# Kernel tuning notes

Measured on AMD Instinct MI355X. Metric: run time of the kernel, lower is better.

The kernel has to match this reference:

```python
import jax, jax.numpy as jnp
import numpy as np

D, N_EXP, N_TOK = 2048, 8, 32768


def setup_inputs() -> dict:
    key = jax.random.key(0)
    k_h, k_eps, k_ww, k_bw, k_wn, k_bn = jax.random.split(key, 6)
    bound = 1.0 / np.sqrt(D)  # nn.Linear default init range
    return {
        "h": jax.random.normal(k_h, (N_TOK, D), dtype=jnp.float32),
        "W_w": jax.random.uniform(k_ww, (D, N_EXP), jnp.float32, -bound, bound),
        "b_w": jax.random.uniform(k_bw, (N_EXP,), jnp.float32, -bound, bound),
        "W_n": jax.random.uniform(k_wn, (D, N_EXP), jnp.float32, -bound, bound),
        "b_n": jax.random.uniform(k_bn, (N_EXP,), jnp.float32, -bound, bound),
        "eps": jax.random.normal(k_eps, (N_TOK, N_EXP), dtype=jnp.float32),
        "top_k": 2,
    }


def reference(h, W_w, b_w, W_n, b_n, eps, top_k):
    # logits = lin_w(h); noise_scale = softplus(lin_noise(h))
    logits = jnp.einsum("td,de->te", h, W_w) + b_w          # [T, E]
    noise = eps * jax.nn.softplus(jnp.einsum("td,de->te", h, W_n) + b_n)
    noisy = logits + noise                                   # [T, E]
    full = jax.nn.softmax(noisy, axis=-1)
    topk_vals, ix = jax.lax.top_k(noisy, top_k)              # [T, k]
    # scatter topk values into -inf tensor == mask non-topk with -inf
    mask = jax.nn.one_hot(ix, noisy.shape[-1], dtype=jnp.bool_).any(axis=-2)  # [T, E]
    sparse = jnp.where(mask, noisy, -jnp.inf)
    return jax.nn.softmax(sparse, axis=-1), ix, full
```

## Files before the change

kernel.cpp:

```cpp
#include <hip/hip_runtime.h>
#include <math.h>

constexpr int D_DIM = 2048;
constexpr int NEXP  = 8;
constexpr int NTOK  = 32768;
constexpr int TT    = 2;
constexpr int SR    = 256;
constexpr int NS    = D_DIM / SR;
constexpr int WPB   = 4;

typedef float vf4 __attribute__((ext_vector_type(4)));
typedef float vf2 __attribute__((ext_vector_type(2)));

__device__ __forceinline__ float softplus_f(float x) {
    return (x > 20.0f) ? x : log1pf(expf(x));
}

__global__ __launch_bounds__(256, 4)
void noisy_topk_router(const float* __restrict__ h,
                       const float* __restrict__ Ww,
                       const float* __restrict__ bw,
                       const float* __restrict__ Wn,
                       const float* __restrict__ bn,
                       const float* __restrict__ eps,
                       float* __restrict__ out_sparse,
                       float* __restrict__ out_ix,
                       float* __restrict__ out_full)
{
    __shared__ vf4 sW4[2048];

    const int tid  = threadIdx.x;
    const int lane = tid & 63;
    const int wave = tid >> 6;
    const int t0   = (blockIdx.x * WPB + wave) * TT;
    const int role = lane & 1;
    const int s7   = lane & 7;

    const float* hbase = h + (size_t)t0 * D_DIM + 4 * lane;

    const int    wm    = (tid >> 3) & 1;
    const int    wfi   = (tid & 7) ^ ((tid >> 4) & 7);
    const float* wbase = (wm ? Wn : Ww) + (tid >> 4) * 32 + wfi * 4;

    vf2 p2[TT * 8];
#pragma unroll
    for (int i = 0; i < TT * 8; ++i) p2[i] = vf2{0.0f, 0.0f};

    vf4 hbuf[2][TT];
    vf4 sreg[4];

#pragma unroll
    for (int k = 0; k < 4; ++k) sreg[k] = *(const vf4*)(wbase + k * 512);
#pragma unroll
    for (int t = 0; t < TT; ++t) hbuf[0][t] = *(const vf4*)(hbase + (size_t)t * D_DIM);
#pragma unroll
    for (int k = 0; k < 4; ++k) sW4[k * 256 + tid] = sreg[k];
    __syncthreads();

#pragma unroll
    for (int S = 0; S < NS; ++S) {
        const int  cur  = S & 1;
        const bool more = (S + 1 < NS);

        if (more) {
#pragma unroll
            for (int k = 0; k < 4; ++k)
                sreg[k] = *(const vf4*)(wbase + (S + 1) * 2048 + k * 512);
#pragma unroll
            for (int t = 0; t < TT; ++t)
                hbuf[cur ^ 1][t] = *(const vf4*)(hbase + (size_t)t * D_DIM + (S + 1) * SR);
        }

        const int Lb = cur * 1024 + lane * 16;
#pragma unroll
        for (int r = 0; r < 4; ++r) {
#pragma unroll
            for (int m = 0; m < 2; ++m) {
                const vf4 w0 = sW4[Lb + ((m * 8 + r * 2 + 0) ^ s7)];
                const vf4 w1 = sW4[Lb + ((m * 8 + r * 2 + 1) ^ s7)];
                const vf2 w0lo = {w0[0], w0[1]}, w0hi = {w0[2], w0[3]};
                const vf2 w1lo = {w1[0], w1[1]}, w1hi = {w1[2], w1[3]};
#pragma unroll
                for (int t = 0; t < TT; ++t) {
                    const float x = hbuf[cur][t][r];
                    const vf2 xx = {x, x};
                    p2[t*8 + m*4 + 0] = __builtin_elementwise_fma(xx, w0lo, p2[t*8 + m*4 + 0]);
                    p2[t*8 + m*4 + 1] = __builtin_elementwise_fma(xx, w0hi, p2[t*8 + m*4 + 1]);
                    p2[t*8 + m*4 + 2] = __builtin_elementwise_fma(xx, w1lo, p2[t*8 + m*4 + 2]);
                    p2[t*8 + m*4 + 3] = __builtin_elementwise_fma(xx, w1hi, p2[t*8 + m*4 + 3]);
                }
            }
        }

        if (more) {
            const int ob = (cur ^ 1) * 1024;
#pragma unroll
            for (int k = 0; k < 4; ++k) sW4[ob + k * 256 + tid] = sreg[k];
            __syncthreads();
        }
    }

    float q[32];
#pragma unroll
    for (int j = 0; j < 32; ++j) {
        const int t = j >> 4, m = j & 1, e = (j >> 2) & 3, el = (j >> 1) & 1;
        q[j] = p2[t*8 + m*4 + e][el];
    }
#pragma unroll
    for (int s = 0; s < 5; ++s) {
        const int mm = 1 << s;
        const bool hi = (lane & mm) != 0;
        const int n = 32 >> (s + 1);
#pragma unroll
        for (int j = 0; j < n; ++j) {
            float a  = q[2 * j];
            float b  = q[2 * j + 1];
            float ta = __shfl_xor(a, mm, 64);
            float tb = __shfl_xor(b, mm, 64);
            q[j] = hi ? (b + tb) : (a + ta);
        }
    }
    const float r0 = q[0] + __shfl_xor(q[0], 32, 64);

    const int  o         = (lane >> 1) & 7;
    const bool noiseLane = (role != 0);
    const int  tok       = t0 + ((lane >> 4) & 1);
    const float bias     = noiseLane ? bn[o] : bw[o];

    const float val = r0 + bias;
    const float sp  = softplus_f(val);
    const float spN = __shfl_xor(sp, 1, 64);
    const float ev  = eps[(size_t)tok * NEXP + o];
    const float noisy = val + ev * spN;

    float v0 = noisy; int i0 = o;
#pragma unroll
    for (int m = 2; m <= 8; m <<= 1) {
        float ov = __shfl_xor(v0, m, 64);
        int   oi = __shfl_xor(i0, m, 64);
        bool take = (ov > v0) || (ov == v0 && oi < i0);
        v0 = take ? ov : v0;
        i0 = take ? oi : i0;
    }
    float v1 = (o == i0) ? -INFINITY : noisy; int i1 = o;
#pragma unroll
    for (int m = 2; m <= 8; m <<= 1) {
        float ov = __shfl_xor(v1, m, 64);
        int   oi = __shfl_xor(i1, m, 64);
        bool take = (ov > v1) || (ov == v1 && oi < i1);
        v1 = take ? ov : v1;
        i1 = take ? oi : i1;
    }
    const float ex = expf(noisy - v0);
    float ssum = ex;
#pragma unroll
    for (int m = 2; m <= 8; m <<= 1) ssum += __shfl_xor(ssum, m, 64);
    const float fullv = ex / ssum;
    const float dd  = expf(v1 - v0);
    const float den = 1.0f + dd;
    const float sparsev = (o == i0) ? (1.0f / den)
                        : (o == i1) ? (dd / den) : 0.0f;

    if (!noiseLane && lane < 32) {
        out_sparse[(size_t)tok * NEXP + o] = sparsev;
        out_full  [(size_t)tok * NEXP + o] = fullv;
        if (o == 0) {
            out_ix[(size_t)tok * 2]     = (float)i0;
            out_ix[(size_t)tok * 2 + 1] = (float)i1;
        }
    }
}

extern "C" void kernel_launch(void* const* d_in, const int* in_sizes, int n_in,
                              void* d_out, int out_size, void* d_ws, size_t ws_size,
                              hipStream_t stream) {
    const float* h   = (const float*)d_in[0];
    const float* Ww  = (const float*)d_in[1];
    const float* bw  = (const float*)d_in[2];
    const float* Wn  = (const float*)d_in[3];
    const float* bn  = (const float*)d_in[4];
    const float* eps = (const float*)d_in[5];

    float* out_sparse = (float*)d_out;
    float* out_ix     = out_sparse + (size_t)NTOK * NEXP;
    float* out_full   = out_ix + (size_t)NTOK * 2;

    const int grid = NTOK / (TT * WPB);
    noisy_topk_router<<<grid, 256, 0, stream>>>(h, Ww, bw, Wn, bn, eps,
                                                out_sparse, out_ix, out_full);
}
```

Measured before the change: 361.1 us.

## Read router weights directly from global memory instead of staging through LDS

Removes the shared-memory double buffer and block-wide barriers used to stage W_w/W_n. Each lane now loads its weight slice straight from global memory (expected to hit L1/L2) with register software prefetch. The h prefetch depth grows from two stages to four, with a sched_barrier to keep the loads issued early. The trade is more global/L1 weight traffic per wave and higher register pressure in exchange for no LDS traffic or __syncthreads.

New measurement: 565.3 us. +56.6%, slower.

```diff
diff --git a/kernel.cpp b/kernel.cpp
--- a/kernel.cpp
+++ b/kernel.cpp
@@ -27,76 +27,70 @@
                        float* __restrict__ out_ix,
                        float* __restrict__ out_full)
 {
-    __shared__ vf4 sW4[2048];
-
     const int tid  = threadIdx.x;
     const int lane = tid & 63;
     const int wave = tid >> 6;
     const int t0   = (blockIdx.x * WPB + wave) * TT;
     const int role = lane & 1;
-    const int s7   = lane & 7;
 
-    const float* hbase = h + (size_t)t0 * D_DIM + 4 * lane;
-
-    const int    wm    = (tid >> 3) & 1;
-    const int    wfi   = (tid & 7) ^ ((tid >> 4) & 7);
-    const float* wbase = (wm ? Wn : Ww) + (tid >> 4) * 32 + wfi * 4;
+    const float* hbase = h  + (size_t)t0 * D_DIM + 4 * lane;
+    const float* ww    = Ww + lane * 32;
+    const float* wn    = Wn + lane * 32;
 
     vf2 p2[TT * 8];
 #pragma unroll
     for (int i = 0; i < TT * 8; ++i) p2[i] = vf2{0.0f, 0.0f};
 
-    vf4 hbuf[2][TT];
-    vf4 sreg[4];
-
+    vf4 hbuf[4][TT];
 #pragma unroll
-    for (int k = 0; k < 4; ++k) sreg[k] = *(const vf4*)(wbase + k * 512);
+    for (int k = 0; k < 3; ++k)
 #pragma unroll
-    for (int t = 0; t < TT; ++t) hbuf[0][t] = *(const vf4*)(hbase + (size_t)t * D_DIM);
-#pragma unroll
-    for (int k = 0; k < 4; ++k) sW4[k * 256 + tid] = sreg[k];
-    __syncthreads();
+        for (int t = 0; t < TT; ++t)
+            hbuf[k][t] = *(const vf4*)(hbase + (size_t)t * D_DIM + k * SR);
 
 #pragma unroll
     for (int S = 0; S < NS; ++S) {
-        const int  cur  = S & 1;
-        const bool more = (S + 1 < NS);
-
-        if (more) {
-#pragma unroll
-            for (int k = 0; k < 4; ++k)
-                sreg[k] = *(const vf4*)(wbase + (S + 1) * 2048 + k * 512);
+        if (S + 3 < NS) {
 #pragma unroll
             for (int t = 0; t < TT; ++t)
-                hbuf[cur ^ 1][t] = *(const vf4*)(hbase + (size_t)t * D_DIM + (S + 1) * SR);
+                hbuf[(S + 3) & 3][t] =
+                    *(const vf4*)(hbase + (size_t)t * D_DIM + (S + 3) * SR);
         }
+        __builtin_amdgcn_sched_barrier(0);
 
-        const int Lb = cur * 1024 + lane * 16;
+        const int soff = S * 2048;
+
+        vf4 ca0 = *(const vf4*)(ww + soff + 0);
+        vf4 ca1 = *(const vf4*)(ww + soff + 4);
+        vf4 cb0 = *(const vf4*)(wn + soff + 0);
+        vf4 cb1 = *(const vf4*)(wn + soff + 4);
 #pragma unroll
         for (int r = 0; r < 4; ++r) {
+            vf4 na0, na1, nb0, nb1;
+            if (r < 3) {
+                na0 = *(const vf4*)(ww + soff + (r + 1) * 8);
+                na1 = *(const vf4*)(ww + soff + (r + 1) * 8 + 4);
+                nb0 = *(const vf4*)(wn + soff + (r + 1) * 8);
+                nb1 = *(const vf4*)(wn + soff + (r + 1) * 8 + 4);
+            }
+            const vf2 a0lo = {ca0[0], ca0[1]}, a0hi = {ca0[2], ca0[3]};
+            const vf2 a1lo = {ca1[0], ca1[1]}, a1hi = {ca1[2], ca1[3]};
+            const vf2 b0lo = {cb0[0], cb0[1]}, b0hi = {cb0[2], cb0[3]};
+            const vf2 b1lo = {cb1[0], cb1[1]}, b1hi = {cb1[2], cb1[3]};
 #pragma unroll
-            for (int m = 0; m < 2; ++m) {
-                const vf4 w0 = sW4[Lb + ((m * 8 + r * 2 + 0) ^ s7)];
-                const vf4 w1 = sW4[Lb + ((m * 8 + r * 2 + 1) ^ s7)];
-                const vf2 w0lo = {w0[0], w0[1]}, w0hi = {w0[2], w0[3]};
-                const vf2 w1lo = {w1[0], w1[1]}, w1hi = {w1[2], w1[3]};
-#pragma unroll
-                for (int t = 0; t < TT; ++t) {
-                    const float x = hbuf[cur][t][r];
-                    const vf2 xx = {x, x};
-                    p2[t*8 + m*4 + 0] = __builtin_elementwise_fma(xx, w0lo, p2[t*8 + m*4 + 0]);
-                    p2[t*8 + m*4 + 1] = __builtin_elementwise_fma(xx, w0hi, p2[t*8 + m*4 + 1]);
-                    p2[t*8 + m*4 + 2] = __builtin_elementwise_fma(xx, w1lo, p2[t*8 + m*4 + 2]);
-                    p2[t*8 + m*4 + 3] = __builtin_elementwise_fma(xx, w1hi, p2[t*8 + m*4 + 3]);
-                }
+            for (int t = 0; t < TT; ++t) {
+                const float x = hbuf[S & 3][t][r];
+                const vf2 xx = {x, x};
+                p2[t*8 + 0] = __builtin_elementwise_fma(xx, a0lo, p2[t*8 + 0]);
+                p2[t*8 + 1] = __builtin_elementwise_fma(xx, a0hi, p2[t*8 + 1]);
+                p2[t*8 + 2] = __builtin_elementwise_fma(xx, a1lo, p2[t*8 + 2]);
+                p2[t*8 + 3] = __builtin_elementwise_fma(xx, a1hi, p2[t*8 + 3]);
+                p2[t*8 + 4] = __builtin_elementwise_fma(xx, b0lo, p2[t*8 + 4]);
+                p2[t*8 + 5] = __builtin_elementwise_fma(xx, b0hi, p2[t*8 + 5]);
+                p2[t*8 + 6] = __builtin_elementwise_fma(xx, b1lo, p2[t*8 + 6]);
+                p2[t*8 + 7] = __builtin_elementwise_fma(xx, b1hi, p2[t*8 + 7]);
             }
-        }
-
-        if (more) {
-            const int ob = (cur ^ 1) * 1024;
-#pragma unroll
-            for (int k = 0; k < 4; ++k) sW4[ob + k * 256 + tid] = sreg[k];
-            __syncthreads();
+            if (r < 3) { ca0 = na0; ca1 = na1; cb0 = nb0; cb1 = nb1; }
         }
     }
 
```

## Load full router weights into LDS once per persistent block

Applied to the files above, without the earlier changes.

Replaces the per-block streaming of weight slices, which was double-buffered through LDS with a barrier per slice, by a persistent grid of 256 blocks of 1024 threads. Each block stages all of W_w and W_n (128 KB dynamic LDS) once and then loops over groups of tokens with no further barriers. This removes the repeated weight reloads and __syncthreads across the 4096 original blocks. In exchange it needs large dynamic shared memory, which limits each CU to one block, and it serializes token groups inside each wave, so occupancy and latency hiding for the h stream may drop.

Result: slower. 881.4 us (+144.1%).

```diff
diff --git a/kernel.cpp b/kernel.cpp
--- a/kernel.cpp
+++ b/kernel.cpp
@@ -1,13 +1,16 @@
 #include <hip/hip_runtime.h>
 #include <math.h>
 
-constexpr int D_DIM = 2048;
-constexpr int NEXP  = 8;
-constexpr int NTOK  = 32768;
-constexpr int TT    = 2;
-constexpr int SR    = 256;
-constexpr int NS    = D_DIM / SR;
-constexpr int WPB   = 4;
+constexpr int D_DIM  = 2048;
+constexpr int NEXP   = 8;
+constexpr int NTOK   = 32768;
+constexpr int TT     = 2;
+constexpr int SR     = 256;
+constexpr int NS     = D_DIM / SR;
+constexpr int WAVES  = 16;
+constexpr int BLKT   = WAVES * 64;
+constexpr int NBLK   = 256;
+constexpr int GROUPS = NTOK / (NBLK * WAVES * TT);
 
 typedef float vf4 __attribute__((ext_vector_type(4)));
 typedef float vf2 __attribute__((ext_vector_type(2)));
@@ -16,7 +19,7 @@
     return (x > 20.0f) ? x : log1pf(expf(x));
 }
 
-__global__ __launch_bounds__(256, 4)
+__global__ __launch_bounds__(1024, 4)
 void noisy_topk_router(const float* __restrict__ h,
                        const float* __restrict__ Ww,
                        const float* __restrict__ bw,
@@ -27,146 +30,146 @@
                        float* __restrict__ out_ix,
                        float* __restrict__ out_full)
 {
-    __shared__ vf4 sW4[2048];
+    extern __shared__ vf4 sW4[];
 
     const int tid  = threadIdx.x;
     const int lane = tid & 63;
     const int wave = tid >> 6;
-    const int t0   = (blockIdx.x * WPB + wave) * TT;
     const int role = lane & 1;
     const int s7   = lane & 7;
 
-    const float* hbase = h + (size_t)t0 * D_DIM + 4 * lane;
-
-    const int    wm    = (tid >> 3) & 1;
-    const int    wfi   = (tid & 7) ^ ((tid >> 4) & 7);
-    const float* wbase = (wm ? Wn : Ww) + (tid >> 4) * 32 + wfi * 4;
-
-    vf2 p2[TT * 8];
-#pragma unroll
-    for (int i = 0; i < TT * 8; ++i) p2[i] = vf2{0.0f, 0.0f};
-
-    vf4 hbuf[2][TT];
-    vf4 sreg[4];
-
-#pragma unroll
-    for (int k = 0; k < 4; ++k) sreg[k] = *(const vf4*)(wbase + k * 512);
-#pragma unroll
-    for (int t = 0; t < TT; ++t) hbuf[0][t] = *(const vf4*)(hbase + (size_t)t * D_DIM);
-#pragma unroll
-    for (int k = 0; k < 4; ++k) sW4[k * 256 + tid] = sreg[k];
+    {
+        const int tt  = tid & 255;
+        const int wm  = (tt >> 3) & 1;
+        const int wfi = (tt & 7) ^ ((tt >> 4) & 7);
+        const float* wsrc = (wm ? Wn : Ww) + (tt >> 4) * 32 + wfi * 4;
+#pragma unroll
+        for (int it = 0; it < 2; ++it) {
+            const int S = (tid >> 8) + it * 4;
+#pragma unroll
+            for (int k = 0; k < 4; ++k) {
+                vf4 v = *(const vf4*)(wsrc + (size_t)S * 2048 + k * 512);
+                sW4[S * 1024 + k * 256 + tt] = v;
+            }
+        }
+    }
     __syncthreads();
 
-#pragma unroll
-    for (int S = 0; S < NS; ++S) {
-        const int  cur  = S & 1;
-        const bool more = (S + 1 < NS);
-
-        if (more) {
-#pragma unroll
-            for (int k = 0; k < 4; ++k)
-                sreg[k] = *(const vf4*)(wbase + (S + 1) * 2048 + k * 512);
-#pragma unroll
-            for (int t = 0; t < TT; ++t)
-                hbuf[cur ^ 1][t] = *(const vf4*)(hbase + (size_t)t * D_DIM + (S + 1) * SR);
-        }
-
-        const int Lb = cur * 1024 + lane * 16;
-#pragma unroll
-        for (int r = 0; r < 4; ++r) {
-#pragma unroll
-            for (int m = 0; m < 2; ++m) {
-                const vf4 w0 = sW4[Lb + ((m * 8 + r * 2 + 0) ^ s7)];
-                const vf4 w1 = sW4[Lb + ((m * 8 + r * 2 + 1) ^ s7)];
-                const vf2 w0lo = {w0[0], w0[1]}, w0hi = {w0[2], w0[3]};
-                const vf2 w1lo = {w1[0], w1[1]}, w1hi = {w1[2], w1[3]};
-#pragma unroll
-                for (int t = 0; t < TT; ++t) {
-                    const float x = hbuf[cur][t][r];
-                    const vf2 xx = {x, x};
-                    p2[t*8 + m*4 + 0] = __builtin_elementwise_fma(xx, w0lo, p2[t*8 + m*4 + 0]);
-                    p2[t*8 + m*4 + 1] = __builtin_elementwise_fma(xx, w0hi, p2[t*8 + m*4 + 1]);
-                    p2[t*8 + m*4 + 2] = __builtin_elementwise_fma(xx, w1lo, p2[t*8 + m*4 + 2]);
-                    p2[t*8 + m*4 + 3] = __builtin_elementwise_fma(xx, w1hi, p2[t*8 + m*4 + 3]);
+#pragma unroll 1
+    for (int g = 0; g < GROUPS; ++g) {
+        const int t0 = blockIdx.x * (WAVES * TT * GROUPS)
+                     + wave * (TT * GROUPS) + g * TT;
+        const float* hbase = h + (size_t)t0 * D_DIM + 4 * lane;
+
+        vf2 p2[TT * 8];
+#pragma unroll
+        for (int i = 0; i < TT * 8; ++i) p2[i] = vf2{0.0f, 0.0f};
+
+        vf4 hbuf[2][TT];
+#pragma unroll
+        for (int t = 0; t < TT; ++t)
+            hbuf[0][t] = *(const vf4*)(hbase + (size_t)t * D_DIM);
+
+#pragma unroll
+        for (int S = 0; S < NS; ++S) {
+            const int cur = S & 1;
+            if (S + 1 < NS) {
+#pragma unroll
+                for (int t = 0; t < TT; ++t)
+                    hbuf[cur ^ 1][t] =
+                        *(const vf4*)(hbase + (size_t)t * D_DIM + (S + 1) * SR);
+            }
+
+            const int Lb = S * 1024 + lane * 16;
+#pragma unroll
+            for (int r = 0; r < 4; ++r) {
+#pragma unroll
+                for (int m = 0; m < 2; ++m) {
+                    const vf4 w0 = sW4[Lb + ((m * 8 + r * 2 + 0) ^ s7)];
+                    const vf4 w1 = sW4[Lb + ((m * 8 + r * 2 + 1) ^ s7)];
+                    const vf2 w0lo = {w0[0], w0[1]}, w0hi = {w0[2], w0[3]};
+                    const vf2 w1lo = {w1[0], w1[1]}, w1hi = {w1[2], w1[3]};
+#pragma unroll
+                    for (int t = 0; t < TT; ++t) {
+                        const float x = hbuf[cur][t][r];
+                        const vf2 xx = {x, x};
+                        p2[t*8 + m*4 + 0] = __builtin_elementwise_fma(xx, w0lo, p2[t*8 + m*4 + 0]);
+                        p2[t*8 + m*4 + 1] = __builtin_elementwise_fma(xx, w0hi, p2[t*8 + m*4 + 1]);
+                        p2[t*8 + m*4 + 2] = __builtin_elementwise_fma(xx, w1lo, p2[t*8 + m*4 + 2]);
+                        p2[t*8 + m*4 + 3] = __builtin_elementwise_fma(xx, w1hi, p2[t*8 + m*4 + 3]);
+                    }
                 }
             }
         }
 
-        if (more) {
-            const int ob = (cur ^ 1) * 1024;
-#pragma unroll
-            for (int k = 0; k < 4; ++k) sW4[ob + k * 256 + tid] = sreg[k];
-            __syncthreads();
-        }
-    }
-
-    float q[32];
-#pragma unroll
-    for (int j = 0; j < 32; ++j) {
-        const int t = j >> 4, m = j & 1, e = (j >> 2) & 3, el = (j >> 1) & 1;
-        q[j] = p2[t*8 + m*4 + e][el];
-    }
-#pragma unroll
-    for (int s = 0; s < 5; ++s) {
-        const int mm = 1 << s;
-        const bool hi = (lane & mm) != 0;
-        const int n = 32 >> (s + 1);
-#pragma unroll
-        for (int j = 0; j < n; ++j) {
-            float a  = q[2 * j];
-            float b  = q[2 * j + 1];
-            float ta = __shfl_xor(a, mm, 64);
-            float tb = __shfl_xor(b, mm, 64);
-            q[j] = hi ? (b + tb) : (a + ta);
-        }
-    }
-    const float r0 = q[0] + __shfl_xor(q[0], 32, 64);
-
-    const int  o         = (lane >> 1) & 7;
-    const bool noiseLane = (role != 0);
-    const int  tok       = t0 + ((lane >> 4) & 1);
-    const float bias     = noiseLane ? bn[o] : bw[o];
-
-    const float val = r0 + bias;
-    const float sp  = softplus_f(val);
-    const float spN = __shfl_xor(sp, 1, 64);
-    const float ev  = eps[(size_t)tok * NEXP + o];
-    const float noisy = val + ev * spN;
-
-    float v0 = noisy; int i0 = o;
-#pragma unroll
-    for (int m = 2; m <= 8; m <<= 1) {
-        float ov = __shfl_xor(v0, m, 64);
-        int   oi = __shfl_xor(i0, m, 64);
-        bool take = (ov > v0) || (ov == v0 && oi < i0);
-        v0 = take ? ov : v0;
-        i0 = take ? oi : i0;
-    }
-    float v1 = (o == i0) ? -INFINITY : noisy; int i1 = o;
-#pragma unroll
-    for (int m = 2; m <= 8; m <<= 1) {
-        float ov = __shfl_xor(v1, m, 64);
-        int   oi = __shfl_xor(i1, m, 64);
-        bool take = (ov > v1) || (ov == v1 && oi < i1);
-        v1 = take ? ov : v1;
-        i1 = take ? oi : i1;
-    }
-    const float ex = expf(noisy - v0);
-    float ssum = ex;
-#pragma unroll
-    for (int m = 2; m <= 8; m <<= 1) ssum += __shfl_xor(ssum, m, 64);
-    const float fullv = ex / ssum;
-    const float dd  = expf(v1 - v0);
-    const float den = 1.0f + dd;
-    const float sparsev = (o == i0) ? (1.0f / den)
-                        : (o == i1) ? (dd / den) : 0.0f;
-
-    if (!noiseLane && lane < 32) {
-        out_sparse[(size_t)tok * NEXP + o] = sparsev;
-        out_full  [(size_t)tok * NEXP + o] = fullv;
-        if (o == 0) {
-            out_ix[(size_t)tok * 2]     = (float)i0;
-            out_ix[(size_t)tok * 2 + 1] = (float)i1;
+        float q[32];
+#pragma unroll
+        for (int j = 0; j < 32; ++j) {
+            const int t = j >> 4, m = j & 1, e = (j >> 2) & 3, el = (j >> 1) & 1;
+            q[j] = p2[t*8 + m*4 + e][el];
+        }
+#pragma unroll
+        for (int s = 0; s < 5; ++s) {
+            const int mm = 1 << s;
+            const bool hi = (lane & mm) != 0;
+            const int n = 32 >> (s + 1);
+#pragma unroll
+            for (int j = 0; j < n; ++j) {
+                float a  = q[2 * j];
+                float b  = q[2 * j + 1];
+                float ta = __shfl_xor(a, mm, 64);
+                float tb = __shfl_xor(b, mm, 64);
+                q[j] = hi ? (b + tb) : (a + ta);
+            }
+        }
+        const float r0 = q[0] + __shfl_xor(q[0], 32, 64);
+
+        const int  o         = (lane >> 1) & 7;
+        const bool noiseLane = (role != 0);
+        const int  tok       = t0 + ((lane >> 4) & 1);
+        const float bias     = noiseLane ? bn[o] : bw[o];
+
+        const float val = r0 + bias;
+        const float sp  = softplus_f(val);
+        const float spN = __shfl_xor(sp, 1, 64);
+        const float ev  = eps[(size_t)tok * NEXP + o];
+        const float noisy = val + ev * spN;
+
+        float v0 = noisy; int i0 = o;
+#pragma unroll
+        for (int m = 2; m <= 8; m <<= 1) {
+            float ov = __shfl_xor(v0, m, 64);
+            int   oi = __shfl_xor(i0, m, 64);
+            bool take = (ov > v0) || (ov == v0 && oi < i0);
+            v0 = take ? ov : v0;
+            i0 = take ? oi : i0;
+        }
+        float v1 = (o == i0) ? -INFINITY : noisy; int i1 = o;
+#pragma unroll
+        for (int m = 2; m <= 8; m <<= 1) {
+            float ov = __shfl_xor(v1, m, 64);
+            int   oi = __shfl_xor(i1, m, 64);
+            bool take = (ov > v1) || (ov == v1 && oi < i1);
+            v1 = take ? ov : v1;
+            i1 = take ? oi : i1;
+        }
+        const float ex = expf(noisy - v0);
+        float ssum = ex;
+#pragma unroll
+        for (int m = 2; m <= 8; m <<= 1) ssum += __shfl_xor(ssum, m, 64);
+        const float fullv = ex / ssum;
+        const float dd  = expf(v1 - v0);
+        const float den = 1.0f + dd;
+        const float sparsev = (o == i0) ? (1.0f / den)
+                            : (o == i1) ? (dd / den) : 0.0f;
+
+        if (!noiseLane && lane < 32) {
+            out_sparse[(size_t)tok * NEXP + o] = sparsev;
+            out_full  [(size_t)tok * NEXP + o] = fullv;
+            if (o == 0) {
+                out_ix[(size_t)tok * 2]     = (float)i0;
+                out_ix[(size_t)tok * 2 + 1] = (float)i1;
+            }
         }
     }
 }
@@ -185,7 +188,13 @@
     float* out_ix     = out_sparse + (size_t)NTOK * NEXP;
     float* out_full   = out_ix + (size_t)NTOK * 2;
 
-    const int grid = NTOK / (TT * WPB);
-    noisy_topk_router<<<grid, 256, 0, stream>>>(h, Ww, bw, Wn, bn, eps,
-                                                out_sparse, out_ix, out_full);
+    static bool attr_done = false;
+    if (!attr_done) {
+        hipFuncSetAttribute((const void*)noisy_topk_router,
+                            hipFuncAttributeMaxDynamicSharedMemorySize,
+                            131072);
+        attr_done = true;
+    }
+    noisy_topk_router<<<NBLK, BLKT, 131072, stream>>>(h, Ww, bw, Wn, bn, eps,
+                                                      out_sparse, out_ix, out_full);
 }
```
